# Kernel tuning notes

Measured on AMD Instinct MI355X. Metric: run time of the kernel, lower is better.

Reference implementation:

```python
import jax, jax.numpy as jnp
import numpy as np

B, N, C_IN = 8, 2048, 3
D = 64            # graph-conv feature dim
SPARSE_K = 8      # k_neighbors(16) * sparse_ratio(0.5)
LEVELS = 3        # wavelet_levels
H1, H2 = 256, 128 # fusion hidden dims

def _lin(key, fan_in, fan_out):
    k1, k2 = jax.random.split(key)
    s = 1.0 / np.sqrt(fan_in)
    W = jax.random.uniform(k1, (fan_in, fan_out), minval=-s, maxval=s, dtype=jnp.float32)
    b = jax.random.uniform(k2, (fan_out,), minval=-s, maxval=s, dtype=jnp.float32)
    return W, b

def setup_inputs() -> dict:
    key = jax.random.key(0)
    ks = jax.random.split(key, 12)
    x = jax.random.normal(ks[0], (B, N, C_IN), dtype=jnp.float32)
    W1, b1 = _lin(ks[1], C_IN, D)          # feature_transform
    W2, b2 = _lin(ks[2], 2 * D, D)         # edge_conv
    Ws1, bs1 = _lin(ks[3], C_IN, 64)       # suppressor layer 1
    Ws2, bs2 = _lin(ks[4], 64, LEVELS)     # suppressor layer 2
    Wf1, bf1 = _lin(ks[5], D * LEVELS, H1) # fusion
    Wf2, bf2 = _lin(ks[6], H1, H2)
    Wf3, bf3 = _lin(ks[7], H2, C_IN)
    ones = jnp.ones; zeros = jnp.zeros
    return {
        'x': x,
        'W1': W1, 'b1': b1, 'g1': ones((D,), jnp.float32), 'be1': zeros((D,), jnp.float32),
        'W2': W2, 'b2': b2, 'g2': ones((D,), jnp.float32), 'be2': zeros((D,), jnp.float32),
        'Ws1': Ws1, 'bs1': bs1, 'Ws2': Ws2, 'bs2': bs2,
        'Wf1': Wf1, 'bf1': bf1, 'gf1': ones((H1,), jnp.float32), 'bef1': zeros((H1,), jnp.float32),
        'Wf2': Wf2, 'bf2': bf2, 'gf2': ones((H2,), jnp.float32), 'bef2': zeros((H2,), jnp.float32),
        'Wf3': Wf3, 'bf3': bf3,
    }

def _leaky(v):
    return jnp.where(v > 0, v, 0.2 * v)

def reference(x, W1, b1, g1, be1, W2, b2, g2, be2, Ws1, bs1, Ws2, bs2,
              Wf1, bf1, gf1, bef1, Wf2, bf2, gf2, bef2, Wf3, bf3):
    # ---- AdaptiveSparseGraphConv ----
    # feature transform + eval-mode BN (running mean 0 / var 1 -> affine)
    feat = _leaky((x @ W1 + b1) * g1 + be1)                     # [B,N,D]
    # KNN via squared distances (monotonic in true cdist)
    x2 = jnp.sum(x * x, axis=-1)                                # [B,N]
    d2 = x2[:, :, None] + x2[:, None, :] - 2.0 * jnp.einsum('bnc,bmc->bnm', x, x)
    _, idx = jax.lax.top_k(-d2, SPARSE_K)                       # [B,N,k] nearest
    neighbor = jax.vmap(lambda f, i: f[i])(feat, idx)           # [B,N,k,D]
    edge = jnp.concatenate(
        [jnp.broadcast_to(feat[:, :, None, :], neighbor.shape), neighbor], axis=-1)  # [B,N,k,2D]
    conv = _leaky((edge @ W2 + b2) * g2 + be2)                  # [B,N,k,D]
    agg = jnp.max(conv, axis=2)                                 # [B,N,D]
    # ---- AdaptiveFrequencySupressor (per-point wavelet-level weights) ----
    fw = jax.nn.sigmoid(jax.nn.relu(x @ Ws1 + bs1) @ Ws2 + bs2) # [B,N,LEVELS]
    # frequency-adaptive multi-level weighting, concat across levels
    multi = (agg[:, :, None, :] * fw[:, :, :, None]).reshape(B, N, LEVELS * D)  # [B,N,LEVELS*D]
    # ---- EnhancedMultiScaleFusion (eval: dropout off, BN affine) ----
    h = _leaky((multi @ Wf1 + bf1) * gf1 + bef1)
    h = _leaky((h @ Wf2 + bf2) * gf2 + bef2)
    delta = h @ Wf3 + bf3                                       # [B,N,3]
    # ---- residual regularized output ----
    return x + 0.1 * delta
```

## Files before the change

### kernel.cpp

```cpp
#include <hip/hip_runtime.h>
#include <hip/hip_bf16.h>
#include <math.h>

#define BB   8
#define NN   2048
#define BN   16384
#define KNB  8

__device__ __forceinline__ float leaky(float v){ return v > 0.f ? v : 0.2f*v; }

__device__ __forceinline__ ushort f2bf(float f){
    unsigned u = __float_as_uint(f);
    return (ushort)((u + 0x7FFFu + ((u >> 16) & 1u)) >> 16);
}
__device__ __forceinline__ float bf2f(ushort h){
    return __uint_as_float(((unsigned)h) << 16);
}

using bf16x8 = __attribute__((ext_vector_type(8))) short;
using f32x16 = __attribute__((ext_vector_type(16))) float;

__global__ __launch_bounds__(256) void k_pq(
    const float* __restrict__ x,
    const float* __restrict__ W1, const float* __restrict__ b1,
    const float* __restrict__ g1, const float* __restrict__ be1,
    const float* __restrict__ W2,
    const float* __restrict__ Wf1, const float* __restrict__ Wf2,
    float* __restrict__ P, ushort* __restrict__ Qb,
    ushort* __restrict__ Wf1T, ushort* __restrict__ Wf2T)
{
    int t = threadIdx.x;
    int bid = blockIdx.x;
    if (bid >= 256) {
        if (bid < 280) {
            int base = (bid - 256) * 2048 + t * 8;
            #pragma unroll
            for (int j = 0; j < 8; ++j) {
                int e = base + j;
                int n = e / 192, k = e % 192;
                Wf1T[e] = f2bf(Wf1[k*256 + n]);
            }
        } else {
            int base = (bid - 280) * 2048 + t * 8;
            #pragma unroll
            for (int j = 0; j < 8; ++j) {
                int e = base + j;
                int n = e / 256, k = e % 256;
                Wf2T[e] = f2bf(Wf2[k*128 + n]);
            }
        }
        return;
    }

    __shared__ float F_s[64*66];
    __shared__ float W_s[32*132];

    int rb = bid * 64;

    {
        int d = t & 63, g = t >> 6;
        float w0 = W1[d], w1 = W1[64+d], w2 = W1[128+d];
        float bb = b1[d], gg = g1[d], ee = be1[d];
        #pragma unroll 4
        for (int i = 0; i < 16; ++i) {
            int r = g*16 + i;
            const float* xp = &x[(rb + r)*3];
            float f = xp[0]*w0 + xp[1]*w1 + xp[2]*w2 + bb;
            f = leaky(f*gg + ee);
            F_s[r*66 + d] = f;
        }
    }

    int tx = t & 15, ty = t >> 4;
    float acc[4][8];
    #pragma unroll
    for (int i = 0; i < 4; ++i)
        #pragma unroll
        for (int j = 0; j < 8; ++j) acc[i][j] = 0.f;

    for (int k0 = 0; k0 < 64; k0 += 32) {
        __syncthreads();
        #pragma unroll
        for (int it = 0; it < 2; ++it) {
            int i2 = t + it*256;
            int k = i2 >> 4, c8 = (i2 & 15) * 8;
            const float* src = &W2[(k0 + k + (c8 >= 64 ? 64 : 0))*64 + (c8 & 63)];
            *(float4*)&W_s[k*132 + c8]     = *(const float4*)src;
            *(float4*)&W_s[k*132 + c8 + 4] = *(const float4*)(src + 4);
        }
        __syncthreads();
        #pragma unroll 4
        for (int kk = 0; kk < 32; ++kk) {
            float a[4];
            #pragma unroll
            for (int i = 0; i < 4; ++i) a[i] = F_s[(ty*4 + i)*66 + k0 + kk];
            float4 wA = *(const float4*)&W_s[kk*132 + tx*8];
            float4 wB = *(const float4*)&W_s[kk*132 + tx*8 + 4];
            #pragma unroll
            for (int i = 0; i < 4; ++i) {
                acc[i][0] = fmaf(a[i], wA.x, acc[i][0]);
                acc[i][1] = fmaf(a[i], wA.y, acc[i][1]);
                acc[i][2] = fmaf(a[i], wA.z, acc[i][2]);
                acc[i][3] = fmaf(a[i], wA.w, acc[i][3]);
                acc[i][4] = fmaf(a[i], wB.x, acc[i][4]);
                acc[i][5] = fmaf(a[i], wB.y, acc[i][5]);
                acc[i][6] = fmaf(a[i], wB.z, acc[i][6]);
                acc[i][7] = fmaf(a[i], wB.w, acc[i][7]);
            }
        }
    }

    #pragma unroll
    for (int i = 0; i < 4; ++i) {
        int r = rb + ty*4 + i;
        if (tx < 8) {
            *(float4*)&P[r*64 + tx*8]     = make_float4(acc[i][0], acc[i][1], acc[i][2], acc[i][3]);
            *(float4*)&P[r*64 + tx*8 + 4] = make_float4(acc[i][4], acc[i][5], acc[i][6], acc[i][7]);
        } else {
            union { ushort u[8]; uint4 v; } pk;
            #pragma unroll
            for (int j = 0; j < 8; ++j) pk.u[j] = f2bf(acc[i][j]);
            *(uint4*)&Qb[r*64 + (tx - 8)*8] = pk.v;
        }
    }
}

#define CE64(a, b) { bool c_ = (b) < (a); unsigned long long mn_ = c_ ? (b) : (a); \
                     unsigned long long mx_ = c_ ? (a) : (b); (a) = mn_; (b) = mx_; }

__global__ __launch_bounds__(1024, 8) void k_knn(const float* __restrict__ x, int* __restrict__ idxo)
{
    __shared__ __align__(16) char smem[65536];
    float4*   sp  = (float4*)smem;
    unsigned* khi = (unsigned*)smem;
    unsigned* klo = (unsigned*)(smem + 32768);

    int t = threadIdx.x;
    int b = blockIdx.x >> 6;
    int qbase = (blockIdx.x & 63) * 32;
    int q = t & 31, seg = t >> 5;

    for (int i = t; i < NN; i += 1024) {
        float a = x[(b*NN + i)*3 + 0];
        float c = x[(b*NN + i)*3 + 1];
        float e = x[(b*NN + i)*3 + 2];
        sp[i] = make_float4(a, c, e, a*a + c*c + e*e);
    }
    __syncthreads();

    float4 qv = sp[qbase + q];

    unsigned long long R[8];
    #pragma unroll
    for (int j = 0; j < 8; ++j) R[j] = 0xFFFFFFFFFFFFFFFFull;

    int m0 = seg * 64;
    #pragma unroll 2
    for (int g = 0; g < 8; ++g) {
        unsigned long long S[8];
        #pragma unroll
        for (int jj = 0; jj < 8; ++jj) {
            int m = m0 + g*8 + jj;
            float4 v = sp[m];
            float s = qv.x*v.x; s = fmaf(qv.y, v.y, s); s = fmaf(qv.z, v.z, s);
            float d2 = fmaf(-2.f, s, qv.w + v.w);
            unsigned u = __float_as_uint(fmaxf(d2, 0.f));
            S[jj] = ((unsigned long long)u << 32) | (unsigned)m;
        }
        CE64(S[0],S[1]); CE64(S[2],S[3]); CE64(S[4],S[5]); CE64(S[6],S[7]);
        CE64(S[0],S[2]); CE64(S[1],S[3]); CE64(S[4],S[6]); CE64(S[5],S[7]);
        CE64(S[1],S[2]); CE64(S[5],S[6]);
        CE64(S[0],S[4]); CE64(S[1],S[5]); CE64(S[2],S[6]); CE64(S[3],S[7]);
        CE64(S[2],S[4]); CE64(S[3],S[5]);
        CE64(S[1],S[2]); CE64(S[3],S[4]); CE64(S[5],S[6]);
        #pragma unroll
        for (int j = 0; j < 8; ++j) {
            unsigned long long bb = S[7-j];
            R[j] = R[j] < bb ? R[j] : bb;
        }
        CE64(R[0],R[4]); CE64(R[1],R[5]); CE64(R[2],R[6]); CE64(R[3],R[7]);
        CE64(R[0],R[2]); CE64(R[1],R[3]); CE64(R[4],R[6]); CE64(R[5],R[7]);
        CE64(R[0],R[1]); CE64(R[2],R[3]); CE64(R[4],R[5]); CE64(R[6],R[7]);
    }

    __syncthreads();
    #pragma unroll
    for (int j = 0; j < 8; ++j) {
        khi[j*1024 + t] = (unsigned)(R[j] >> 32);
        klo[j*1024 + t] = (unsigned)R[j];
    }

    for (int L = 32; L >= 2; L >>= 1) {
        __syncthreads();
        unsigned long long A[8], Bv[8];
        int p = t >> 5;
        bool active = (p < (L >> 1));
        if (active) {
            int rowA = (2*p)*32 + q, rowB = (2*p + 1)*32 + q;
            #pragma unroll
            for (int j = 0; j < 8; ++j) {
                A[j]  = ((unsigned long long)khi[j*1024 + rowA] << 32) | klo[j*1024 + rowA];
                Bv[j] = ((unsigned long long)khi[j*1024 + rowB] << 32) | klo[j*1024 + rowB];
            }
        }
        __syncthreads();
        if (active) {
            unsigned long long C[8];
            #pragma unroll
            for (int j = 0; j < 8; ++j) {
                unsigned long long bb = Bv[7-j];
                C[j] = A[j] < bb ? A[j] : bb;
            }
            CE64(C[0],C[4]); CE64(C[1],C[5]); CE64(C[2],C[6]); CE64(C[3],C[7]);
            CE64(C[0],C[2]); CE64(C[1],C[3]); CE64(C[4],C[6]); CE64(C[5],C[7]);
            CE64(C[0],C[1]); CE64(C[2],C[3]); CE64(C[4],C[5]); CE64(C[6],C[7]);
            if (L > 2) {
                int rowO = p*32 + q;
                #pragma unroll
                for (int j = 0; j < 8; ++j) {
                    khi[j*1024 + rowO] = (unsigned)(C[j] >> 32);
                    klo[j*1024 + rowO] = (unsigned)C[j];
                }
            } else {
                #pragma unroll
                for (int j = 0; j < 8; ++j)
                    idxo[(b*NN + qbase + q)*KNB + j] = b*NN + (int)(C[j] & 0xFFFFFFFFu);
            }
        }
    }
}

__global__ __launch_bounds__(256) void k_fuse(
    const float* __restrict__ x,
    const float* __restrict__ P, const ushort* __restrict__ Qb,
    const int* __restrict__ idx,
    const float* __restrict__ Ws1, const float* __restrict__ bs1,
    const float* __restrict__ Ws2, const float* __restrict__ bs2,
    const float* __restrict__ b2, const float* __restrict__ g2,
    const float* __restrict__ be2,
    const ushort* __restrict__ Wf1T, const float* __restrict__ bf1,
    const float* __restrict__ gf1, const float* __restrict__ bef1,
    const ushort* __restrict__ Wf2T, const float* __restrict__ bf2,
    const float* __restrict__ gf2, const float* __restrict__ bef2,
    const float* __restrict__ Wf3, const float* __restrict__ bf3,
    float* __restrict__ out)
{
    __shared__ __align__(16) char smem[60928];
    ushort* A_s  = (ushort*)smem;
    ushort* B_s  = (ushort*)(smem + 25600);
    ushort* h1_s = (ushort*)smem;
    ushort* B2_s = (ushort*)(smem + 40960);
    float*  pd   = (float*) (smem + 59392);

    int t = threadIdx.x, w = t >> 6, lane = t & 63;
    int rb = blockIdx.x * 64;

    {
        float ws1a = Ws1[lane], ws1b = Ws1[64+lane], ws1c = Ws1[128+lane];
        float bs1v = bs1[lane];
        float ws2a = Ws2[lane*3+0], ws2b = Ws2[lane*3+1], ws2c = Ws2[lane*3+2];
        float bs20 = bs2[0], bs21 = bs2[1], bs22 = bs2[2];
        float g2v = g2[lane], be2v = be2[lane], b2v = b2[lane];
        for (int i = 0; i < 16; ++i) {
            int r = w*16 + i, p = rb + r;
            float x0 = x[p*3+0], x1 = x[p*3+1], x2 = x[p*3+2];
            float h = fmaxf(fmaf(x2, ws1c, fmaf(x1, ws1b, fmaf(x0, ws1a, bs1v))), 0.f);
            float s0 = h*ws2a, s1 = h*ws2b, s2 = h*ws2c;
            #pragma unroll
            for (int off = 32; off; off >>= 1) {
                s0 += __shfl_xor(s0, off, 64);
                s1 += __shfl_xor(s1, off, 64);
                s2 += __shfl_xor(s2, off, 64);
            }
            float fw0 = 1.f/(1.f + expf(-(s0 + bs20)));
            float fw1 = 1.f/(1.f + expf(-(s1 + bs21)));
            float fw2 = 1.f/(1.f + expf(-(s2 + bs22)));
            float Pv = P[p*64 + lane] + b2v;
            float mx = -1e30f;
            #pragma unroll
            for (int j = 0; j < KNB; ++j) {
                int nb = idx[p*KNB + j];
                float qv = bf2f(Qb[nb*64 + lane]);
                mx = fmaxf(mx, leaky((Pv + qv)*g2v + be2v));
            }
            A_s[r*200 + lane]       = f2bf(mx * fw0);
            A_s[r*200 + 64 + lane]  = f2bf(mx * fw1);
            A_s[r*200 + 128 + lane] = f2bf(mx * fw2);
        }
    }

    int rg = w >> 1;
    int nh = (w & 1) * 128;
    int l31 = lane & 31, kb = (lane >> 5) * 8;
    int row = rg*32 + l31;

    f32x16 acc[4];
    #pragma unroll
    for (int n2 = 0; n2 < 4; ++n2)
        #pragma unroll
        for (int i = 0; i < 16; ++i) acc[n2][i] = 0.f;

    for (int k0 = 0; k0 < 192; k0 += 64) {
        __syncthreads();
        #pragma unroll
        for (int it = 0; it < 8; ++it) {
            int i = t + it*256;
            int n = i >> 3, kq = (i & 7)*8;
            *(uint4*)&B_s[n*72 + kq] = *(const uint4*)&Wf1T[n*192 + k0 + kq];
        }
        __syncthreads();
        #pragma unroll
        for (int s = 0; s < 4; ++s) {
            bf16x8 a = *(const bf16x8*)&A_s[row*200 + k0 + s*16 + kb];
            #pragma unroll
            for (int n2 = 0; n2 < 4; ++n2) {
                bf16x8 b = *(const bf16x8*)&B_s[(nh + n2*32 + l31)*72 + s*16 + kb];
                acc[n2] = __builtin_amdgcn_mfma_f32_32x32x16_bf16(a, b, acc[n2], 0, 0, 0);
            }
        }
    }
    __syncthreads();

    #pragma unroll
    for (int n2 = 0; n2 < 4; ++n2) {
        int c = nh + n2*32 + l31;
        float bv = bf1[c], gv = gf1[c], ev = bef1[c];
        #pragma unroll
        for (int r16 = 0; r16 < 16; ++r16) {
            int rr = (r16 & 3) + 8*(r16 >> 2) + 4*(lane >> 5);
            float v = leaky((acc[n2][r16] + bv)*gv + ev);
            h1_s[(rg*32 + rr)*264 + c] = f2bf(v);
        }
    }

    int ch = (w & 1) * 64;
    f32x16 acc2[2];
    #pragma unroll
    for (int n2 = 0; n2 < 2; ++n2)
        #pragma unroll
        for (int i = 0; i < 16; ++i) acc2[n2][i] = 0.f;

    for (int k0 = 0; k0 < 256; k0 += 64) {
        __syncthreads();
        #pragma unroll
        for (int it = 0; it < 4; ++it) {
            int i = t + it*256;
            int n = i >> 3, kq = (i & 7)*8;
            *(uint4*)&B2_s[n*72 + kq] = *(const uint4*)&Wf2T[n*256 + k0 + kq];
        }
        __syncthreads();
        #pragma unroll
        for (int s = 0; s < 4; ++s) {
            bf16x8 a = *(const bf16x8*)&h1_s[row*264 + k0 + s*16 + kb];
            #pragma unroll
            for (int n2 = 0; n2 < 2; ++n2) {
                bf16x8 b = *(const bf16x8*)&B2_s[(ch + n2*32 + l31)*72 + s*16 + kb];
                acc2[n2] = __builtin_amdgcn_mfma_f32_32x32x16_bf16(a, b, acc2[n2], 0, 0, 0);
            }
        }
    }

    float bv[2], gv[2], ev[2], w3[2][3];
    #pragma unroll
    for (int n2 = 0; n2 < 2; ++n2) {
        int c = ch + n2*32 + l31;
        bv[n2] = bf2[c]; gv[n2] = gf2[c]; ev[n2] = bef2[c];
        #pragma unroll
        for (int l = 0; l < 3; ++l) w3[n2][l] = Wf3[c*3 + l];
    }
    __syncthreads();
    #pragma unroll
    for (int r16 = 0; r16 < 16; ++r16) {
        float d0 = 0.f, d1 = 0.f, d2 = 0.f;
        #pragma unroll
        for (int n2 = 0; n2 < 2; ++n2) {
            float v = leaky((acc2[n2][r16] + bv[n2])*gv[n2] + ev[n2]);
            d0 = fmaf(v, w3[n2][0], d0);
            d1 = fmaf(v, w3[n2][1], d1);
            d2 = fmaf(v, w3[n2][2], d2);
        }
        #pragma unroll
        for (int off = 16; off; off >>= 1) {
            d0 += __shfl_xor(d0, off, 64);
            d1 += __shfl_xor(d1, off, 64);
            d2 += __shfl_xor(d2, off, 64);
        }
        int rr = rg*32 + (r16 & 3) + 8*(r16 >> 2) + 4*(lane >> 5);
        if (l31 < 3) {
            float dl = (l31 == 0) ? d0 : (l31 == 1 ? d1 : d2);
            pd[(rr*2 + (w & 1))*3 + l31] = dl;
        }
    }
    __syncthreads();

    if (t < 192) {
        int r = t / 3, l = t - r*3;
        float delta = pd[(r*2 + 0)*3 + l] + pd[(r*2 + 1)*3 + l] + bf3[l];
        out[(rb + r)*3 + l] = x[(rb + r)*3 + l] + 0.1f*delta;
    }
}

extern "C" void kernel_launch(void* const* d_in, const int* in_sizes, int n_in,
                              void* d_out, int out_size, void* d_ws, size_t ws_size,
                              hipStream_t stream)
{
    const float* x    = (const float*)d_in[0];
    const float* W1   = (const float*)d_in[1];
    const float* b1   = (const float*)d_in[2];
    const float* g1   = (const float*)d_in[3];
    const float* be1  = (const float*)d_in[4];
    const float* W2   = (const float*)d_in[5];
    const float* b2   = (const float*)d_in[6];
    const float* g2   = (const float*)d_in[7];
    const float* be2  = (const float*)d_in[8];
    const float* Ws1  = (const float*)d_in[9];
    const float* bs1  = (const float*)d_in[10];
    const float* Ws2  = (const float*)d_in[11];
    const float* bs2  = (const float*)d_in[12];
    const float* Wf1  = (const float*)d_in[13];
    const float* bf1  = (const float*)d_in[14];
    const float* gf1  = (const float*)d_in[15];
    const float* bef1 = (const float*)d_in[16];
    const float* Wf2  = (const float*)d_in[17];
    const float* bf2  = (const float*)d_in[18];
    const float* gf2  = (const float*)d_in[19];
    const float* bef2 = (const float*)d_in[20];
    const float* Wf3  = (const float*)d_in[21];
    const float* bf3  = (const float*)d_in[22];
    float* out = (float*)d_out;

    char* ws = (char*)d_ws;
    int*    idx   = (int*)   (ws + 0);
    ushort* Wf1T  = (ushort*)(ws + (1u << 20));
    ushort* Wf2T  = (ushort*)(ws + (1u << 20) + (512u << 10));
    float*  P     = (float*) (ws + (2u  << 20));
    ushort* Qb    = (ushort*)(ws + (6u  << 20));

    k_pq<<<296, 256, 0, stream>>>(x, W1, b1, g1, be1, W2, Wf1, Wf2, P, Qb, Wf1T, Wf2T);
    k_knn<<<BB*64, 1024, 0, stream>>>(x, idx);
    k_fuse<<<BN/64, 256, 0, stream>>>(x, P, Qb, idx, Ws1, bs1, Ws2, bs2, b2, g2, be2,
                                      Wf1T, bf1, gf1, bef1, Wf2T, bf2, gf2, bef2,
                                      Wf3, bf3, out);
}
```

Measured before the change: 172.1 us.

## Replace 64-bit key/index KNN sort with float-only threshold then ballot index recovery

The KNN kernel now keeps only float distances in its sorting networks instead of packed 64-bit distance|index keys, which halves register and LDS traffic per compare-exchange. The first merge level uses a cross-half wavefront shuffle instead of shared memory. The 8th-smallest distance becomes a threshold. A second pass recomputes all distances and uses ballots and popcounts to emit indices below the threshold, then fills ties from an equal-value buffer. This adds a full second distance scan per query, and the neighbour order inside each output row is now by index rather than by distance. That order does not matter because the results are max-aggregated.

```diff
diff --git a/kernel.cpp b/kernel.cpp
--- a/kernel.cpp
+++ b/kernel.cpp
@@ -125,20 +125,22 @@
     }
 }
 
-#define CE64(a, b) { bool c_ = (b) < (a); unsigned long long mn_ = c_ ? (b) : (a); \
-                     unsigned long long mx_ = c_ ? (a) : (b); (a) = mn_; (b) = mx_; }
+#define CEF(a, b) { float mn_ = fminf(a,b), mx_ = fmaxf(a,b); (a) = mn_; (b) = mx_; }
 
 __global__ __launch_bounds__(1024, 8) void k_knn(const float* __restrict__ x, int* __restrict__ idxo)
 {
-    __shared__ __align__(16) char smem[65536];
-    float4*   sp  = (float4*)smem;
-    unsigned* khi = (unsigned*)smem;
-    unsigned* klo = (unsigned*)(smem + 32768);
+    __shared__ __align__(16) char smem[50560];
+    float4* sp    = (float4*)smem;
+    float*  mg    = (float*) (smem + 32768);
+    float*  v8buf = (float*) (smem + 49152);
+    int*    eqbuf = (int*)   (smem + 49280);
+    int*    c1buf = (int*)   (smem + 50304);
 
     int t = threadIdx.x;
     int b = blockIdx.x >> 6;
     int qbase = (blockIdx.x & 63) * 32;
     int q = t & 31, seg = t >> 5;
+    int w = t >> 6, lane = t & 63;
 
     for (int i = t; i < NN; i += 1024) {
         float a = x[(b*NN + i)*3 + 0];
@@ -149,84 +151,122 @@
     __syncthreads();
 
     float4 qv = sp[qbase + q];
-
-    unsigned long long R[8];
-    #pragma unroll
-    for (int j = 0; j < 8; ++j) R[j] = 0xFFFFFFFFFFFFFFFFull;
+    float R[8];
+    #pragma unroll
+    for (int j = 0; j < 8; ++j) R[j] = 1e30f;
 
     int m0 = seg * 64;
     #pragma unroll 2
     for (int g = 0; g < 8; ++g) {
-        unsigned long long S[8];
+        float S[8];
         #pragma unroll
         for (int jj = 0; jj < 8; ++jj) {
             int m = m0 + g*8 + jj;
             float4 v = sp[m];
             float s = qv.x*v.x; s = fmaf(qv.y, v.y, s); s = fmaf(qv.z, v.z, s);
             float d2 = fmaf(-2.f, s, qv.w + v.w);
-            unsigned u = __float_as_uint(fmaxf(d2, 0.f));
-            S[jj] = ((unsigned long long)u << 32) | (unsigned)m;
-        }
-        CE64(S[0],S[1]); CE64(S[2],S[3]); CE64(S[4],S[5]); CE64(S[6],S[7]);
-        CE64(S[0],S[2]); CE64(S[1],S[3]); CE64(S[4],S[6]); CE64(S[5],S[7]);
-        CE64(S[1],S[2]); CE64(S[5],S[6]);
-        CE64(S[0],S[4]); CE64(S[1],S[5]); CE64(S[2],S[6]); CE64(S[3],S[7]);
-        CE64(S[2],S[4]); CE64(S[3],S[5]);
-        CE64(S[1],S[2]); CE64(S[3],S[4]); CE64(S[5],S[6]);
-        #pragma unroll
-        for (int j = 0; j < 8; ++j) {
-            unsigned long long bb = S[7-j];
-            R[j] = R[j] < bb ? R[j] : bb;
-        }
-        CE64(R[0],R[4]); CE64(R[1],R[5]); CE64(R[2],R[6]); CE64(R[3],R[7]);
-        CE64(R[0],R[2]); CE64(R[1],R[3]); CE64(R[4],R[6]); CE64(R[5],R[7]);
-        CE64(R[0],R[1]); CE64(R[2],R[3]); CE64(R[4],R[5]); CE64(R[6],R[7]);
-    }
-
-    __syncthreads();
-    #pragma unroll
-    for (int j = 0; j < 8; ++j) {
-        khi[j*1024 + t] = (unsigned)(R[j] >> 32);
-        klo[j*1024 + t] = (unsigned)R[j];
-    }
-
-    for (int L = 32; L >= 2; L >>= 1) {
-        __syncthreads();
-        unsigned long long A[8], Bv[8];
-        int p = t >> 5;
-        bool active = (p < (L >> 1));
+            S[jj] = fmaxf(d2, 0.f);
+        }
+        CEF(S[0],S[1]); CEF(S[2],S[3]); CEF(S[4],S[5]); CEF(S[6],S[7]);
+        CEF(S[0],S[2]); CEF(S[1],S[3]); CEF(S[4],S[6]); CEF(S[5],S[7]);
+        CEF(S[1],S[2]); CEF(S[5],S[6]);
+        CEF(S[0],S[4]); CEF(S[1],S[5]); CEF(S[2],S[6]); CEF(S[3],S[7]);
+        CEF(S[2],S[4]); CEF(S[3],S[5]);
+        CEF(S[1],S[2]); CEF(S[3],S[4]); CEF(S[5],S[6]);
+        #pragma unroll
+        for (int j = 0; j < 8; ++j) R[j] = fminf(R[j], S[7-j]);
+        CEF(R[0],R[4]); CEF(R[1],R[5]); CEF(R[2],R[6]); CEF(R[3],R[7]);
+        CEF(R[0],R[2]); CEF(R[1],R[3]); CEF(R[4],R[6]); CEF(R[5],R[7]);
+        CEF(R[0],R[1]); CEF(R[2],R[3]); CEF(R[4],R[5]); CEF(R[6],R[7]);
+    }
+
+    {
+        float Rp[8];
+        #pragma unroll
+        for (int j = 0; j < 8; ++j) Rp[j] = __shfl_xor(R[j], 32, 64);
+        float C[8];
+        #pragma unroll
+        for (int j = 0; j < 8; ++j) C[j] = fminf(R[j], Rp[7-j]);
+        CEF(C[0],C[4]); CEF(C[1],C[5]); CEF(C[2],C[6]); CEF(C[3],C[7]);
+        CEF(C[0],C[2]); CEF(C[1],C[3]); CEF(C[4],C[6]); CEF(C[5],C[7]);
+        CEF(C[0],C[1]); CEF(C[2],C[3]); CEF(C[4],C[5]); CEF(C[6],C[7]);
+        if (lane < 32) {
+            #pragma unroll
+            for (int j = 0; j < 8; ++j) mg[(w*32 + lane)*8 + j] = C[j];
+        }
+    }
+
+    #pragma unroll
+    for (int lvl = 0; lvl < 4; ++lvl) {
+        int P = 8 >> lvl;
+        int sh = 3 - lvl;
+        bool active = (t < 32*P);
+        float C[8];
+        int qq = 0, p = 0;
+        __syncthreads();
         if (active) {
-            int rowA = (2*p)*32 + q, rowB = (2*p + 1)*32 + q;
+            qq = t >> sh; p = t & (P - 1);
+            float A[8], Bv[8];
             #pragma unroll
             for (int j = 0; j < 8; ++j) {
-                A[j]  = ((unsigned long long)khi[j*1024 + rowA] << 32) | klo[j*1024 + rowA];
-                Bv[j] = ((unsigned long long)khi[j*1024 + rowB] << 32) | klo[j*1024 + rowB];
-            }
+                A[j]  = mg[((2*p)*32 + qq)*8 + j];
+                Bv[j] = mg[((2*p + 1)*32 + qq)*8 + j];
+            }
+            #pragma unroll
+            for (int j = 0; j < 8; ++j) C[j] = fminf(A[j], Bv[7-j]);
+            CEF(C[0],C[4]); CEF(C[1],C[5]); CEF(C[2],C[6]); CEF(C[3],C[7]);
+            CEF(C[0],C[2]); CEF(C[1],C[3]); CEF(C[4],C[6]); CEF(C[5],C[7]);
+            CEF(C[0],C[1]); CEF(C[2],C[3]); CEF(C[4],C[5]); CEF(C[6],C[7]);
         }
         __syncthreads();
         if (active) {
-            unsigned long long C[8];
-            #pragma unroll
-            for (int j = 0; j < 8; ++j) {
-                unsigned long long bb = Bv[7-j];
-                C[j] = A[j] < bb ? A[j] : bb;
-            }
-            CE64(C[0],C[4]); CE64(C[1],C[5]); CE64(C[2],C[6]); CE64(C[3],C[7]);
-            CE64(C[0],C[2]); CE64(C[1],C[3]); CE64(C[4],C[6]); CE64(C[5],C[7]);
-            CE64(C[0],C[1]); CE64(C[2],C[3]); CE64(C[4],C[5]); CE64(C[6],C[7]);
-            if (L > 2) {
-                int rowO = p*32 + q;
+            if (P > 1) {
                 #pragma unroll
-                for (int j = 0; j < 8; ++j) {
-                    khi[j*1024 + rowO] = (unsigned)(C[j] >> 32);
-                    klo[j*1024 + rowO] = (unsigned)C[j];
+                for (int j = 0; j < 8; ++j) mg[(p*32 + qq)*8 + j] = C[j];
+            } else {
+                v8buf[qq] = C[7];
+            }
+        }
+    }
+    __syncthreads();
+
+    #pragma unroll
+    for (int u = 0; u < 2; ++u) {
+        int qq = w*2 + u;
+        float4 qv2 = sp[qbase + qq];
+        float v8 = v8buf[qq];
+        int cLT = 0, cEQ = 0;
+        unsigned long long below = (1ull << lane) - 1ull;
+        for (int g = 0; g < 32; ++g) {
+            int m = g*64 + lane;
+            float4 v = sp[m];
+            float s = qv2.x*v.x; s = fmaf(qv2.y, v.y, s); s = fmaf(qv2.z, v.z, s);
+            float d2 = fmaf(-2.f, s, qv2.w + v.w);
+            d2 = fmaxf(d2, 0.f);
+            bool lt = d2 < v8, eq = d2 == v8;
+            unsigned long long mlt = __ballot(lt);
+            unsigned long long meq = __ballot(eq);
+            if (mlt | meq) {
+                if (lt) {
+                    int r = cLT + __popcll(mlt & below);
+                    if (r < 8) idxo[(b*NN + qbase + qq)*KNB + r] = b*NN + m;
+                } else if (eq) {
+                    int r = cEQ + __popcll(meq & below);
+                    if (r < 8) eqbuf[qq*8 + r] = m;
                 }
-            } else {
-                #pragma unroll
-                for (int j = 0; j < 8; ++j)
-                    idxo[(b*NN + qbase + q)*KNB + j] = b*NN + (int)(C[j] & 0xFFFFFFFFu);
-            }
-        }
+                cLT += (int)__popcll(mlt);
+                cEQ += (int)__popcll(meq);
+            }
+        }
+        if (lane == 0) c1buf[qq] = cLT < 8 ? cLT : 8;
+    }
+    __syncthreads();
+
+    if (t < 256) {
+        int qq = t >> 3, j = t & 7;
+        int c1 = c1buf[qq];
+        if (j >= c1)
+            idxo[(b*NN + qbase + qq)*KNB + j] = b*NN + eqbuf[qq*8 + (j - c1)];
     }
 }
 
```

Result: faster. 163.2 us (-5.2%).
